# Kernel optimization log

Measured on AMD Instinct MI355X. Metric: run time of the kernel, lower is better.

The kernel has to match this reference:

```python
import jax, jax.numpy as jnp
import numpy as np

N = 131072
K = 27
FIN = 3
FOUT = 32
EPS = 1e-5


def _bn(h, gamma, beta, mean, var):
    return (h - mean) * jax.lax.rsqrt(var + EPS) * gamma + beta


def setup_inputs() -> dict:
    key = jax.random.key(0)
    ks = jax.random.split(key, 8)
    return {
        "x_feats": jax.random.normal(ks[0], (N, FIN), jnp.float32),
        "z_feats": jax.random.normal(ks[1], (N, FIN), jnp.float32),
        "nbr_idx": jax.random.randint(ks[2], (N, K), 0, N, jnp.int32),
        "w1": jax.random.normal(ks[3], (K, FIN, FOUT), jnp.float32) * 0.2,
        "bn1_gamma": jnp.ones((FOUT,), jnp.float32),
        "bn1_beta": jnp.zeros((FOUT,), jnp.float32),
        "bn1_mean": jax.random.normal(ks[4], (FOUT,), jnp.float32) * 0.1,
        "bn1_var": jax.random.uniform(ks[5], (FOUT,), jnp.float32, 0.5, 1.5),
        "w2": jax.random.normal(ks[6], (K, FOUT, FOUT), jnp.float32) * 0.1,
        "mlp_w": jax.random.normal(ks[7], (FIN, FOUT), jnp.float32) * 0.3,
        "mlp_b": jnp.zeros((FOUT,), jnp.float32),
        "mlp_gamma": jnp.ones((FOUT,), jnp.float32),
        "mlp_beta": jnp.zeros((FOUT,), jnp.float32),
        "mlp_mean": jnp.zeros((FOUT,), jnp.float32),
        "mlp_var": jnp.ones((FOUT,), jnp.float32),
    }


def reference(x_feats, z_feats, nbr_idx, w1, bn1_gamma, bn1_beta, bn1_mean,
              bn1_var, w2, mlp_w, mlp_b, mlp_gamma, mlp_beta, mlp_mean,
              mlp_var):
    # --- voxel branch: sparse conv (gather-GEMM) -> BN -> SiLU -> sparse conv
    g1 = x_feats[nbr_idx]                       # [N, K, FIN] irregular gather
    h = jnp.einsum('nkf,kfo->no', g1, w1)       # [N, FOUT]
    h = jax.nn.silu(_bn(h, bn1_gamma, bn1_beta, bn1_mean, bn1_var))
    g2 = h[nbr_idx]                             # [N, K, FOUT] irregular gather
    x_out = jnp.einsum('nkf,kfo->no', g2, w2)   # [N, FOUT]

    # --- point branch: SharedMLP = Linear -> BN -> ReLU
    z = z_feats @ mlp_w + mlp_b
    z = jax.nn.relu(_bn(z, mlp_gamma, mlp_beta, mlp_mean, mlp_var))

    # --- mixed_mix: fuse voxel and point features additively
    fused = x_out + z
    return (fused, fused)
```

## Files before the change

### kernel.cpp

```cpp
#include <hip/hip_runtime.h>
#include <math.h>

#define NN 131072
#define KK 27
#define FIN 3
#define FOUT 32
#define EPS 1e-5f

typedef _Float16 f16;
typedef __attribute__((ext_vector_type(8))) _Float16 f16x8;
typedef __attribute__((ext_vector_type(16))) float f32x16;

__global__ __launch_bounds__(256) void pack_x_kernel(
    const float* __restrict__ x, float4* __restrict__ xp)
{
    const int n = blockIdx.x * 256 + threadIdx.x;
    if (n < NN)
        xp[n] = make_float4(x[n * 3], x[n * 3 + 1], x[n * 3 + 2], 0.f);
}

__global__ __launch_bounds__(256) void pack_w2_kernel(
    const float* __restrict__ w2, f16* __restrict__ w2p)
{
    const int t = blockIdx.x * 256 + threadIdx.x;
    if (t >= KK * 2 * 64 * 8) return;
    const int k    = t >> 10;
    const int rem  = t & 1023;
    const int half = rem >> 9;
    const int l    = (rem >> 3) & 63;
    const int j    = rem & 7;
    const int krow = half * 16 + ((l >> 5) << 3) + j;
    const int n    = l & 31;
    w2p[t] = (f16)w2[k * (FOUT * FOUT) + krow * FOUT + n];
}

__global__ __launch_bounds__(256) void conv1_kernel(
    const float4* __restrict__ xp,
    const int*   __restrict__ nbr_idx,
    const float* __restrict__ w1,
    const float* __restrict__ g1,  const float* __restrict__ b1,
    const float* __restrict__ m1,  const float* __restrict__ v1,
    f16* __restrict__ h_out)
{
    __shared__ float4 xs[64 * KK];

    const int tid  = threadIdx.x;
    const int nb0  = blockIdx.x * 64;

    const int* nb = nbr_idx + (size_t)nb0 * KK;
    {
        int   idxv[7];
        float4 xv[7];
#pragma unroll
        for (int t = 0; t < 7; ++t) {
            const int i = t * 256 + tid;
            idxv[t] = (i < 64 * KK) ? nb[i] : 0;
        }
#pragma unroll
        for (int t = 0; t < 7; ++t)
            xv[t] = xp[idxv[t]];
#pragma unroll
        for (int t = 0; t < 7; ++t) {
            const int i = t * 256 + tid;
            if (i < 64 * KK) xs[i] = xv[t];
        }
    }
    __syncthreads();

    const int l  = tid & 63;
    const int ob = __builtin_amdgcn_readfirstlane((tid >> 6) * 8);

    float acc[8];
#pragma unroll
    for (int o = 0; o < 8; ++o) acc[o] = 0.f;

#pragma unroll 9
    for (int k = 0; k < KK; ++k) {
        const float4 xv = xs[l * KK + k];
        const float* w = w1 + k * (FIN * FOUT) + ob;
#pragma unroll
        for (int o = 0; o < 8; ++o) {
            float a = acc[o];
            a = fmaf(xv.x, w[o],            a);
            a = fmaf(xv.y, w[FOUT + o],     a);
            a = fmaf(xv.z, w[2 * FOUT + o], a);
            acc[o] = a;
        }
    }

    f16x8 hv;
#pragma unroll
    for (int j = 0; j < 8; ++j) {
        const int o = ob + j;
        const float sc = g1[o] * rsqrtf(v1[o] + EPS);
        float v = (acc[j] - m1[o]) * sc + b1[o];
        v = v / (1.f + __expf(-v));
        hv[j] = (f16)v;
    }
    *(f16x8*)(h_out + (size_t)(nb0 + l) * FOUT + ob) = hv;
}

__global__ __launch_bounds__(256) void conv2_mfma_kernel(
    const f16*   __restrict__ h,
    const int*   __restrict__ nbr_idx,
    const f16*   __restrict__ w2p,
    const float* __restrict__ z_feats,
    const float* __restrict__ mlp_w,
    const float* __restrict__ mlp_b,
    const float* __restrict__ mg, const float* __restrict__ mbe,
    const float* __restrict__ mm, const float* __restrict__ mv,
    float* __restrict__ out)
{
    const int lane = threadIdx.x & 63;
    const int wave = threadIdx.x >> 6;
    const int base = (blockIdx.x * 4 + wave) * 32;
    const int row  = lane & 31;
    const int hi   = lane >> 5;

    int idxs[KK];
    const int* nb = nbr_idx + (size_t)(base + row) * KK;
#pragma unroll
    for (int k = 0; k < KK; ++k) idxs[k] = nb[k];

    f32x16 acc = {};

    const f16x8* bp = (const f16x8*)w2p;
#pragma unroll 3
    for (int k = 0; k < KK; ++k) {
        const f16* hr = h + (size_t)idxs[k] * FOUT + hi * 8;
        const f16x8 a1 = *(const f16x8*)hr;
        const f16x8 a2 = *(const f16x8*)(hr + 16);
        const f16x8 b1 = bp[k * 128 + lane];
        const f16x8 b2 = bp[k * 128 + 64 + lane];
        acc = __builtin_amdgcn_mfma_f32_32x32x16_f16(a1, b1, acc, 0, 0, 0);
        acc = __builtin_amdgcn_mfma_f32_32x32x16_f16(a2, b2, acc, 0, 0, 0);
    }

    const int n0 = lane & 31;
    const float wc0 = mlp_w[n0];
    const float wc1 = mlp_w[FOUT + n0];
    const float wc2 = mlp_w[2 * FOUT + n0];
    const float sc  = mg[n0] * rsqrtf(mv[n0] + EPS);
    const float bi  = mlp_b[n0];
    const float mmv = mm[n0];
    const float mbv = mbe[n0];

#pragma unroll
    for (int r = 0; r < 16; ++r) {
        const int m    = (r & 3) + ((r >> 2) << 3) + (hi << 2);
        const int node = base + m;
        const float* zr = z_feats + (size_t)node * FIN;
        float z = bi;
        z = fmaf(zr[0], wc0, z);
        z = fmaf(zr[1], wc1, z);
        z = fmaf(zr[2], wc2, z);
        z = (z - mmv) * sc + mbv;
        z = fmaxf(z, 0.f);
        const float v = acc[r] + z;
        out[(size_t)node * FOUT + n0] = v;
        out[(size_t)NN * FOUT + (size_t)node * FOUT + n0] = v;
    }
}

extern "C" void kernel_launch(void* const* d_in, const int* in_sizes, int n_in,
                              void* d_out, int out_size, void* d_ws, size_t ws_size,
                              hipStream_t stream) {
    const float* x_feats = (const float*)d_in[0];
    const float* z_feats = (const float*)d_in[1];
    const int*   nbr_idx = (const int*)d_in[2];
    const float* w1      = (const float*)d_in[3];
    const float* bn1_g   = (const float*)d_in[4];
    const float* bn1_b   = (const float*)d_in[5];
    const float* bn1_m   = (const float*)d_in[6];
    const float* bn1_v   = (const float*)d_in[7];
    const float* w2      = (const float*)d_in[8];
    const float* mlp_w   = (const float*)d_in[9];
    const float* mlp_b   = (const float*)d_in[10];
    const float* mlp_g   = (const float*)d_in[11];
    const float* mlp_be  = (const float*)d_in[12];
    const float* mlp_m   = (const float*)d_in[13];
    const float* mlp_v   = (const float*)d_in[14];

    f16*    h   = (f16*)d_ws;
    f16*    w2p = (f16*)((char*)d_ws + (size_t)8 * 1024 * 1024);
    float4* xp  = (float4*)((char*)d_ws + (size_t)9 * 1024 * 1024);
    float*  out = (float*)d_out;

    pack_x_kernel<<<NN / 256, 256, 0, stream>>>(x_feats, xp);
    pack_w2_kernel<<<(KK * 1024 + 255) / 256, 256, 0, stream>>>(w2, w2p);
    conv1_kernel<<<NN / 64, 256, 0, stream>>>(xp, nbr_idx, w1,
                                              bn1_g, bn1_b, bn1_m, bn1_v, h);
    conv2_mfma_kernel<<<NN / 128, 256, 0, stream>>>(h, nbr_idx, w2p, z_feats,
                                                    mlp_w, mlp_b, mlp_g, mlp_be,
                                                    mlp_m, mlp_v, out);
}
```

Baseline: 172.6 us.

## Stage conv2 weights in LDS and software-pipeline neighbor gathers in chunks

The conv2 MFMA kernel now copies the packed w2 weights into shared memory, padded to 28 taps with a zero tap, so each block reads them once from global memory. The 27 neighbor gathers are split into four chunks of seven, and the next chunk's gathers are issued before the current chunk's MFMAs run, so gather latency overlaps with compute. The cost is 56 KB of LDS per block and a large register footprint for the double-buffered A fragments, which may lower occupancy. The padded tap also performs one extra zero-weight MFMA pair per wave.

```diff
diff --git a/kernel.cpp b/kernel.cpp
--- a/kernel.cpp
+++ b/kernel.cpp
@@ -3,6 +3,7 @@
 
 #define NN 131072
 #define KK 27
+#define KP 28
 #define FIN 3
 #define FOUT 32
 #define EPS 1e-5f
@@ -23,7 +24,7 @@
     const float* __restrict__ w2, f16* __restrict__ w2p)
 {
     const int t = blockIdx.x * 256 + threadIdx.x;
-    if (t >= KK * 2 * 64 * 8) return;
+    if (t >= KP * 1024) return;
     const int k    = t >> 10;
     const int rem  = t & 1023;
     const int half = rem >> 9;
@@ -31,7 +32,7 @@
     const int j    = rem & 7;
     const int krow = half * 16 + ((l >> 5) << 3) + j;
     const int n    = l & 31;
-    w2p[t] = (f16)w2[k * (FOUT * FOUT) + krow * FOUT + n];
+    w2p[t] = (k < KK) ? (f16)w2[k * (FOUT * FOUT) + krow * FOUT + n] : (f16)0.f;
 }
 
 __global__ __launch_bounds__(256) void conv1_kernel(
@@ -49,7 +50,7 @@
 
     const int* nb = nbr_idx + (size_t)nb0 * KK;
     {
-        int   idxv[7];
+        int    idxv[7];
         float4 xv[7];
 #pragma unroll
         for (int t = 0; t < 7; ++t) {
@@ -111,29 +112,63 @@
     const float* __restrict__ mm, const float* __restrict__ mv,
     float* __restrict__ out)
 {
-    const int lane = threadIdx.x & 63;
-    const int wave = threadIdx.x >> 6;
+    __shared__ f16 lb[KP * 1024];
+
+    const int tid = threadIdx.x;
+
+    {
+        const float4* src = (const float4*)w2p;
+        float4* dst = (float4*)lb;
+#pragma unroll
+        for (int t = 0; t < 14; ++t)
+            dst[t * 256 + tid] = src[t * 256 + tid];
+    }
+    __syncthreads();
+
+    const int lane = tid & 63;
+    const int wave = tid >> 6;
     const int base = (blockIdx.x * 4 + wave) * 32;
     const int row  = lane & 31;
     const int hi   = lane >> 5;
 
-    int idxs[KK];
+    int idxs[KP];
     const int* nb = nbr_idx + (size_t)(base + row) * KK;
 #pragma unroll
     for (int k = 0; k < KK; ++k) idxs[k] = nb[k];
+    idxs[KK] = 0;
 
     f32x16 acc = {};
-
-    const f16x8* bp = (const f16x8*)w2p;
-#pragma unroll 3
-    for (int k = 0; k < KK; ++k) {
-        const f16* hr = h + (size_t)idxs[k] * FOUT + hi * 8;
-        const f16x8 a1 = *(const f16x8*)hr;
-        const f16x8 a2 = *(const f16x8*)(hr + 16);
-        const f16x8 b1 = bp[k * 128 + lane];
-        const f16x8 b2 = bp[k * 128 + 64 + lane];
-        acc = __builtin_amdgcn_mfma_f32_32x32x16_f16(a1, b1, acc, 0, 0, 0);
-        acc = __builtin_amdgcn_mfma_f32_32x32x16_f16(a2, b2, acc, 0, 0, 0);
+    const f16x8* lbp = (const f16x8*)lb;
+
+    f16x8 A1[7], A2[7];
+#pragma unroll
+    for (int t = 0; t < 7; ++t) {
+        const f16* hr = h + (size_t)idxs[t] * FOUT + hi * 8;
+        A1[t] = *(const f16x8*)hr;
+        A2[t] = *(const f16x8*)(hr + 16);
+    }
+
+#pragma unroll
+    for (int c = 0; c < 4; ++c) {
+        f16x8 N1[7], N2[7];
+        if (c < 3) {
+#pragma unroll
+            for (int t = 0; t < 7; ++t) {
+                const f16* hr = h + (size_t)idxs[(c + 1) * 7 + t] * FOUT + hi * 8;
+                N1[t] = *(const f16x8*)hr;
+                N2[t] = *(const f16x8*)(hr + 16);
+            }
+        }
+#pragma unroll
+        for (int t = 0; t < 7; ++t) {
+            const int k = c * 7 + t;
+            const f16x8 b1 = lbp[k * 128 + lane];
+            const f16x8 b2 = lbp[k * 128 + 64 + lane];
+            acc = __builtin_amdgcn_mfma_f32_32x32x16_f16(A1[t], b1, acc, 0, 0, 0);
+            acc = __builtin_amdgcn_mfma_f32_32x32x16_f16(A2[t], b2, acc, 0, 0, 0);
+        }
+#pragma unroll
+        for (int t = 0; t < 7; ++t) { A1[t] = N1[t]; A2[t] = N2[t]; }
     }
 
     const int n0 = lane & 31;
@@ -187,7 +222,7 @@
     float*  out = (float*)d_out;
 
     pack_x_kernel<<<NN / 256, 256, 0, stream>>>(x_feats, xp);
-    pack_w2_kernel<<<(KK * 1024 + 255) / 256, 256, 0, stream>>>(w2, w2p);
+    pack_w2_kernel<<<(KP * 1024 + 255) / 256, 256, 0, stream>>>(w2, w2p);
     conv1_kernel<<<NN / 64, 256, 0, stream>>>(xp, nbr_idx, w1,
                                               bn1_g, bn1_b, bn1_m, bn1_v, h);
     conv2_mfma_kernel<<<NN / 128, 256, 0, stream>>>(h, nbr_idx, w2p, z_feats,
```

New measurement: 178.6 us. 1.03x slower.
